# Kernel optimization log

Measured on AMD Instinct MI355X. Metric: run time of the kernel, lower is better.

The kernel has to match this reference:

```python
import jax, jax.numpy as jnp
import numpy as np

N = 50000          # nodes
E = 600000         # edges
D_IN = 256         # input_feat_dim
H1 = 128           # hidden_dim1
H2 = 64            # hidden_dim2
DK = 64            # trs_depth (total key/value depth)
HEADS = 2


def setup_inputs() -> dict:
    key = jax.random.key(0)
    ks = jax.random.split(key, 12)
    inp = {
        "ns_emb": jax.random.normal(ks[0], (N, D_IN), dtype=jnp.float32),
        "edge_rows": jax.random.randint(ks[1], (E,), 0, N, dtype=jnp.int32),
        "edge_cols": jax.random.randint(ks[2], (E,), 0, N, dtype=jnp.int32),
        "edge_vals": jax.random.uniform(ks[3], (E,), dtype=jnp.float32),
        "condition": jax.random.normal(ks[4], (1, 128, H1), dtype=jnp.float32),
        # GCN linear weights (bias=False), stored [in, out]
        "W_hidden": jax.random.normal(ks[5], (D_IN, H1), dtype=jnp.float32) / np.sqrt(D_IN),
        "W_mu": jax.random.normal(ks[6], (H1, H2), dtype=jnp.float32) / np.sqrt(H1),
        "W_var": jax.random.normal(ks[7], (H1, H2), dtype=jnp.float32) / np.sqrt(H1),
        # MultiHeadAttention (bias-free) projections
        "Wq": jax.random.normal(ks[8], (H1, DK), dtype=jnp.float32) / np.sqrt(H1),
        "Wk": jax.random.normal(ks[9], (H1, DK), dtype=jnp.float32) / np.sqrt(H1),
        "Wv": jax.random.normal(ks[10], (H1, DK), dtype=jnp.float32) / np.sqrt(H1),
        "Wo": jax.random.normal(ks[11], (DK, H1), dtype=jnp.float32) / np.sqrt(DK),
    }
    return inp


def _spmm(rows, cols, vals, x):
    # sparse [N,N] @ x  via gather + segment-sum over COO edges
    gathered = vals[:, None] * x[cols]            # [E, d]
    return jax.ops.segment_sum(gathered, rows, num_segments=N)


def _gcn(x, W, rows, cols, vals):
    # dropout is identity in eval mode
    support = jax.nn.leaky_relu(x @ W)            # [N, out]
    out = _spmm(rows, cols, vals, support)        # [N, out]
    return jax.nn.leaky_relu(out)


def _mha(q, kv, Wq, Wk, Wv, Wo):
    # MoEL-style MultiHeadAttention, bias-free, no mask/dropout
    B, Lq, _ = q.shape
    Lk = kv.shape[1]
    dk = DK // HEADS
    Q = (q @ Wq).reshape(B, Lq, HEADS, dk).transpose(0, 2, 1, 3) * (dk ** -0.5)
    K = (kv @ Wk).reshape(B, Lk, HEADS, dk).transpose(0, 2, 1, 3)
    V = (kv @ Wv).reshape(B, Lk, HEADS, dk).transpose(0, 2, 1, 3)
    logits = jnp.einsum("bhqd,bhkd->bhqk", Q, K)
    w = jax.nn.softmax(logits, axis=-1)
    ctx = jnp.einsum("bhqk,bhkd->bhqd", w, V)
    ctx = ctx.transpose(0, 2, 1, 3).reshape(B, Lq, DK)
    return ctx @ Wo, w


def reference(ns_emb, edge_rows, edge_cols, edge_vals, condition,
              W_hidden, W_mu, W_var, Wq, Wk, Wv, Wo):
    hidden = _gcn(ns_emb, W_hidden, edge_rows, edge_cols, edge_vals)   # [N, H1]
    attended, _ = _mha(hidden[None], condition, Wq, Wk, Wv, Wo)        # [1, N, H1]
    h = attended[0]
    mu = _gcn(h, W_mu, edge_rows, edge_cols, edge_vals)                # [N, H2]
    var = _gcn(h, W_var, edge_rows, edge_cols, edge_vals)              # [N, H2]
    return mu, var
```

## Files before the change

kernel.cpp:

```cpp
#include <hip/hip_runtime.h>
#include <hip/hip_bf16.h>
#include <cstdint>


typedef __attribute__((ext_vector_type(8))) short short8;
typedef __attribute__((ext_vector_type(4))) float f32x4;

__device__ __forceinline__ unsigned short f2bf(float f) {
    unsigned int u = __builtin_bit_cast(unsigned int, f);
    u += 0x7fffu + ((u >> 16) & 1u);
    return (unsigned short)(u >> 16);
}
__device__ __forceinline__ float bf2f(unsigned short v) {
    return __builtin_bit_cast(float, (unsigned int)v << 16);
}
__device__ __forceinline__ unsigned int pk2(float a, float b) {
    unsigned int r;
    asm("v_cvt_pk_bf16_f32 %0, %1, %2" : "=v"(r) : "v"(a), "v"(b));
    return r;
}


__global__ __launch_bounds__(256) void hist_prep_kernel(
    const int* __restrict__ rows, int* __restrict__ cnt, int E, int HB,
    const float* __restrict__ Wh, const float* __restrict__ Wq,
    const float* __restrict__ cond,
    const float* __restrict__ Wk, const float* __restrict__ Wv,
    const float* __restrict__ Wo, const float* __restrict__ Wmu,
    const float* __restrict__ Wvar,
    unsigned short* __restrict__ WhT, unsigned short* __restrict__ WqT,
    unsigned short* __restrict__ Ktt, unsigned short* __restrict__ Vt,
    unsigned short* __restrict__ WomT)
{
    const int t = threadIdx.x;
    if ((int)blockIdx.x < HB) {
        int i = blockIdx.x * 256 + t;
        if (i < E) atomicAdd(&cnt[rows[i]], 1);
        return;
    }
    const int bid = blockIdx.x - HB;
    if (bid < 160) {
        int idx = bid * 256 + t;
        if (idx < 32768) {
            int n = idx & 127, k = idx >> 7;
            WhT[n * 256 + k] = f2bf(Wh[k * 128 + n]);
        } else {
            int i = idx - 32768, n = i & 63, k = i >> 6;
            WqT[n * 128 + k] = f2bf(Wq[k * 64 + n]);
        }
    } else if (bid < 224) {
        int b2 = bid - 160;
        __shared__ float c[2][128];
        c[t >> 7][t & 127] = cond[b2 * 256 + t];
        __syncthreads();
        int j = b2 * 2 + (t >> 7);
        int tl = t & 127;
        const float* W = (tl < 64) ? Wk : Wv;
        int col = tl & 63;
        float acc = 0.f;
#pragma unroll 8
        for (int k = 0; k < 128; ++k) acc = fmaf(c[t >> 7][k], W[k * 64 + col], acc);
        int h = col >> 5, d = col & 31;
        if (tl < 64) Ktt[((size_t)h * 128 + j) * 32 + d] = f2bf(acc * 0.17677669529663687f);
        else         Vt[((size_t)h * 32 + d) * 128 + j] = f2bf(acc);
    } else {
        int wb = bid - 224;
        __shared__ float WoTl[128 * 65];
#pragma unroll
        for (int i = 0; i < 32; ++i) {
            int idx = t + 256 * i;
            int d = idx >> 7, k = idx & 127;
            WoTl[k * 65 + d] = Wo[idx];
        }
        __syncthreads();
        int o = wb * 256 + t;
        int d = o & 63, n = o >> 6;
        const float* W = (n < 64) ? Wmu : Wvar;
        int j = n & 63;
        float acc = 0.f;
#pragma unroll 8
        for (int k = 0; k < 128; ++k) acc = fmaf(WoTl[k * 65 + d], W[k * 64 + j], acc);
        WomT[n * 64 + d] = f2bf(acc);
    }
}


__global__ __launch_bounds__(256) void scan_fused_kernel(
    const int* __restrict__ cnt, int* __restrict__ bsum, int* __restrict__ flag,
    int* __restrict__ row_start, int* __restrict__ cursor, int N, int E)
{
    __shared__ int sh[256];
    const int t = threadIdx.x, b = blockIdx.x;
    const int i = b * 256 + t;
    int v = (i < N) ? cnt[i] : 0;
    sh[t] = v;
    __syncthreads();
    for (int off = 1; off < 256; off <<= 1) {
        int x = (t >= off) ? sh[t - off] : 0;
        __syncthreads();
        sh[t] += x;
        __syncthreads();
    }
    const int incl = sh[t];
    const int aggregate = sh[255];

    if (t == 255) {
        __hip_atomic_store(&bsum[b], aggregate, __ATOMIC_RELAXED, __HIP_MEMORY_SCOPE_AGENT);
        __hip_atomic_store(&flag[b], 1, __ATOMIC_RELEASE, __HIP_MEMORY_SCOPE_AGENT);
    }

    int acc = 0;
    if (t < b) {
        while (__hip_atomic_load(&flag[t], __ATOMIC_ACQUIRE, __HIP_MEMORY_SCOPE_AGENT) == 0) {}
        acc = __hip_atomic_load(&bsum[t], __ATOMIC_RELAXED, __HIP_MEMORY_SCOPE_AGENT);
    }
    __syncthreads();
    sh[t] = acc;
    __syncthreads();
    for (int off = 128; off > 0; off >>= 1) {
        if (t < off) sh[t] += sh[t + off];
        __syncthreads();
    }
    const int boff = sh[0];
    if (i < N) {
        int w = incl - v + boff;
        row_start[i] = w;
        cursor[i] = w;
    }
    if (b == 0 && t == 0) row_start[N] = E;
}

__global__ void scatter_kernel(const int* __restrict__ rows, const int* __restrict__ colsIn,
                               const float* __restrict__ valsIn, int* __restrict__ cursor,
                               int2* __restrict__ pack, int E) {
    int i = blockIdx.x * blockDim.x + threadIdx.x;
    if (i < E) {
        int r = rows[i];
        int p = atomicAdd(&cursor[r], 1);
        pack[p] = make_int2(colsIn[i], __float_as_int(valsIn[i]));
    }
}


__global__ __launch_bounds__(256) void gcn1_gemm(
    const float* __restrict__ A, const unsigned short* __restrict__ BT,
    unsigned short* __restrict__ C, int M)
{
    __shared__ unsigned short As[128][72];
    __shared__ unsigned short Bs[128][72];

    const int tid = threadIdx.x;
    const int lane = tid & 63, wave = tid >> 6;
    const int wm = wave & 1, wn = wave >> 1;
    const int quad = lane >> 4, l16 = lane & 15;
    const int r0 = blockIdx.x * 128;

    f32x4 acc[4][4];
#pragma unroll
    for (int mt = 0; mt < 4; ++mt)
#pragma unroll
        for (int nt = 0; nt < 4; ++nt)
#pragma unroll
            for (int r = 0; r < 4; ++r) acc[mt][nt][r] = 0.f;

    for (int kc = 0; kc < 256; kc += 64) {
#pragma unroll
        for (int i = 0; i < 8; ++i) {
            int f = tid + 256 * i;
            int row = f >> 4, kq = (f & 15) << 2;
            int gr = r0 + row;
            if (gr >= M) gr = M - 1;
            float4 v = *reinterpret_cast<const float4*>(&A[(size_t)gr * 256 + kc + kq]);
            unsigned int lo = pk2(v.x, v.y), hi = pk2(v.z, v.w);
            *reinterpret_cast<uint2*>(&As[row][kq]) = make_uint2(lo, hi);
        }
#pragma unroll
        for (int i = 0; i < 4; ++i) {
            int f = tid + 256 * i;
            int n = f >> 3, k8 = (f & 7) << 3;
            *reinterpret_cast<short8*>(&Bs[n][k8]) =
                *reinterpret_cast<const short8*>(&BT[(size_t)n * 256 + kc + k8]);
        }
        __syncthreads();

#pragma unroll
        for (int ks = 0; ks < 2; ++ks) {
            const int koff = ks * 32 + quad * 8;
            short8 a[4], b[4];
#pragma unroll
            for (int mt = 0; mt < 4; ++mt)
                a[mt] = *reinterpret_cast<const short8*>(&As[wm * 64 + mt * 16 + l16][koff]);
#pragma unroll
            for (int nt = 0; nt < 4; ++nt)
                b[nt] = *reinterpret_cast<const short8*>(&Bs[wn * 64 + nt * 16 + l16][koff]);
#pragma unroll
            for (int mt = 0; mt < 4; ++mt)
#pragma unroll
                for (int nt = 0; nt < 4; ++nt)
                    acc[mt][nt] = __builtin_amdgcn_mfma_f32_16x16x32_bf16(
                        a[mt], b[nt], acc[mt][nt], 0, 0, 0);
        }
        __syncthreads();
    }

#pragma unroll
    for (int mt = 0; mt < 4; ++mt)
#pragma unroll
        for (int nt = 0; nt < 4; ++nt) {
            int gc = wn * 64 + nt * 16 + l16;
#pragma unroll
            for (int r = 0; r < 4; ++r) {
                int gr = r0 + wm * 64 + mt * 16 + quad * 4 + r;
                if (gr < M) {
                    float v = acc[mt][nt][r];
                    v = v > 0.f ? v : 0.01f * v;
                    C[(size_t)gr * 128 + gc] = f2bf(v);
                }
            }
        }
}


__global__ __launch_bounds__(256) void attn_muvar_kernel(
    const unsigned short* __restrict__ hidden,
    const unsigned short* __restrict__ WqT,
    const unsigned short* __restrict__ Ktt,
    const unsigned short* __restrict__ Vt,
    const unsigned short* __restrict__ WomT,
    unsigned short* __restrict__ muvar,
    int M)
{
    __shared__ unsigned short Qs[4][16 * 72];
    __shared__ unsigned short Ps[4][16 * 136];
    __shared__ unsigned short Csh[4][16 * 72];

    const int tid = threadIdx.x;
    const int lane = tid & 63, wave = tid >> 6;
    const int quad = lane >> 4, l16 = lane & 15;

    const int strip = blockIdx.x * 4 + wave;
    const int base = strip * 16;
    if (base >= M) return;
    int qrow = base + l16;
    if (qrow >= M) qrow = M - 1;

    unsigned short* Q  = &Qs[wave][0];
    unsigned short* P  = &Ps[wave][0];
    unsigned short* Cl = &Csh[wave][0];

    {
        f32x4 qacc[4];
#pragma unroll
        for (int mt = 0; mt < 4; ++mt)
#pragma unroll
            for (int r = 0; r < 4; ++r) qacc[mt][r] = 0.f;

        short8 hb[4];
#pragma unroll
        for (int ks = 0; ks < 4; ++ks)
            hb[ks] = *reinterpret_cast<const short8*>(
                &hidden[(size_t)qrow * 128 + ks * 32 + quad * 8]);
#pragma unroll
        for (int mt = 0; mt < 4; ++mt)
#pragma unroll
            for (int ks = 0; ks < 4; ++ks) {
                short8 a = *reinterpret_cast<const short8*>(
                    &WqT[(size_t)(mt * 16 + l16) * 128 + ks * 32 + quad * 8]);
                qacc[mt] = __builtin_amdgcn_mfma_f32_16x16x32_bf16(a, hb[ks], qacc[mt], 0, 0, 0);
            }
#pragma unroll
        for (int mt = 0; mt < 4; ++mt) {
            uint2 w;
            w.x = pk2(qacc[mt][0], qacc[mt][1]);
            w.y = pk2(qacc[mt][2], qacc[mt][3]);
            *reinterpret_cast<uint2*>(&Q[l16 * 72 + mt * 16 + quad * 4]) = w;
        }
    }

    f32x4 ctv[2][2];
#pragma unroll
    for (int h = 0; h < 2; ++h)
#pragma unroll
        for (int mt = 0; mt < 2; ++mt)
#pragma unroll
            for (int r = 0; r < 4; ++r) ctv[h][mt][r] = 0.f;

#pragma unroll
    for (int h = 0; h < 2; ++h) {
        f32x4 st[8];
        short8 qb = *reinterpret_cast<const short8*>(&Q[l16 * 72 + h * 32 + quad * 8]);
#pragma unroll
        for (int mt = 0; mt < 8; ++mt) {
            short8 a = *reinterpret_cast<const short8*>(
                &Ktt[(size_t)h * 4096 + (mt * 16 + l16) * 32 + quad * 8]);
            f32x4 z; z[0] = 0.f; z[1] = 0.f; z[2] = 0.f; z[3] = 0.f;
            st[mt] = __builtin_amdgcn_mfma_f32_16x16x32_bf16(a, qb, z, 0, 0, 0);
        }

        float mx = st[0][0];
#pragma unroll
        for (int mt = 0; mt < 8; ++mt)
#pragma unroll
            for (int r = 0; r < 4; ++r) mx = fmaxf(mx, st[mt][r]);
        mx = fmaxf(mx, __shfl_xor(mx, 16, 64));
        mx = fmaxf(mx, __shfl_xor(mx, 32, 64));
        float s = 0.f;
#pragma unroll
        for (int mt = 0; mt < 8; ++mt)
#pragma unroll
            for (int r = 0; r < 4; ++r) {
                float e = __expf(st[mt][r] - mx);
                st[mt][r] = e;
                s += e;
            }
        s += __shfl_xor(s, 16, 64);
        s += __shfl_xor(s, 32, 64);
        float inv = 1.0f / s;

#pragma unroll
        for (int mt = 0; mt < 8; ++mt) {
            uint2 w;
            w.x = pk2(st[mt][0] * inv, st[mt][1] * inv);
            w.y = pk2(st[mt][2] * inv, st[mt][3] * inv);
            *reinterpret_cast<uint2*>(&P[l16 * 136 + mt * 16 + quad * 4]) = w;
        }

#pragma unroll
        for (int ks = 0; ks < 4; ++ks) {
            short8 pb = *reinterpret_cast<const short8*>(&P[l16 * 136 + ks * 32 + quad * 8]);
#pragma unroll
            for (int mt = 0; mt < 2; ++mt) {
                short8 a = *reinterpret_cast<const short8*>(
                    &Vt[(size_t)h * 4096 + (mt * 16 + l16) * 128 + ks * 32 + quad * 8]);
                ctv[h][mt] = __builtin_amdgcn_mfma_f32_16x16x32_bf16(a, pb, ctv[h][mt], 0, 0, 0);
            }
        }
    }

#pragma unroll
    for (int h = 0; h < 2; ++h)
#pragma unroll
        for (int mt = 0; mt < 2; ++mt) {
            uint2 w;
            w.x = pk2(ctv[h][mt][0], ctv[h][mt][1]);
            w.y = pk2(ctv[h][mt][2], ctv[h][mt][3]);
            *reinterpret_cast<uint2*>(&Cl[l16 * 72 + h * 32 + mt * 16 + quad * 4]) = w;
        }

    {
        f32x4 mv[8];
#pragma unroll
        for (int mt = 0; mt < 8; ++mt)
#pragma unroll
            for (int r = 0; r < 4; ++r) mv[mt][r] = 0.f;
        short8 cb[2];
#pragma unroll
        for (int ks = 0; ks < 2; ++ks)
            cb[ks] = *reinterpret_cast<const short8*>(&Cl[l16 * 72 + ks * 32 + quad * 8]);
#pragma unroll
        for (int mt = 0; mt < 8; ++mt)
#pragma unroll
            for (int ks = 0; ks < 2; ++ks) {
                short8 a = *reinterpret_cast<const short8*>(
                    &WomT[(size_t)(mt * 16 + l16) * 64 + ks * 32 + quad * 8]);
                mv[mt] = __builtin_amdgcn_mfma_f32_16x16x32_bf16(a, cb[ks], mv[mt], 0, 0, 0);
            }
        if (base + l16 < M) {
#pragma unroll
            for (int mt = 0; mt < 8; ++mt) {
                float v0 = mv[mt][0], v1 = mv[mt][1], v2 = mv[mt][2], v3 = mv[mt][3];
                v0 = v0 > 0.f ? v0 : 0.01f * v0;
                v1 = v1 > 0.f ? v1 : 0.01f * v1;
                v2 = v2 > 0.f ? v2 : 0.01f * v2;
                v3 = v3 > 0.f ? v3 : 0.01f * v3;
                uint2 w;
                w.x = pk2(v0, v1);
                w.y = pk2(v2, v3);
                *reinterpret_cast<uint2*>(
                    &muvar[(size_t)(base + l16) * 128 + mt * 16 + quad * 4]) = w;
            }
        }
    }
}


template<bool SPLIT, typename OT>
__global__ __launch_bounds__(256) void spmm_kernel(
    const int* __restrict__ row_start, const int2* __restrict__ pack,
    const unsigned short* __restrict__ X,
    OT* __restrict__ out0, OT* __restrict__ out1, int N)
{
    const int wave = threadIdx.x >> 6, lane = threadIdx.x & 63;
    const int r = blockIdx.x * 4 + wave;
    if (r >= N) return;
    const int s = __builtin_amdgcn_readfirstlane(row_start[r]);
    const int e = __builtin_amdgcn_readfirstlane(row_start[r + 1]);
    const int fo = lane * 2;

    float ax[16], ay[16];
#pragma unroll
    for (int k = 0; k < 16; ++k) { ax[k] = 0.f; ay[k] = 0.f; }

    for (int i = s; i < e; i += 16) {
        int2 p[16];
        unsigned int x[16];
#pragma unroll
        for (int k = 0; k < 16; ++k) {
            int idx = i + k;
            p[k] = pack[idx < e ? idx : e - 1];
        }
#pragma unroll
        for (int k = 0; k < 16; ++k)
            x[k] = *reinterpret_cast<const unsigned int*>(&X[(size_t)p[k].x * 128 + fo]);
#pragma unroll
        for (int k = 0; k < 16; ++k) {
            float v = (i + k < e) ? __int_as_float(p[k].y) : 0.f;
            ax[k] = fmaf(v, bf2f((unsigned short)x[k]), ax[k]);
            ay[k] = fmaf(v, bf2f((unsigned short)(x[k] >> 16)), ay[k]);
        }
    }

    float ox = (((ax[0] + ax[1]) + (ax[2] + ax[3])) + ((ax[4] + ax[5]) + (ax[6] + ax[7]))) +
               (((ax[8] + ax[9]) + (ax[10] + ax[11])) + ((ax[12] + ax[13]) + (ax[14] + ax[15])));
    float oy = (((ay[0] + ay[1]) + (ay[2] + ay[3])) + ((ay[4] + ay[5]) + (ay[6] + ay[7]))) +
               (((ay[8] + ay[9]) + (ay[10] + ay[11])) + ((ay[12] + ay[13]) + (ay[14] + ay[15])));
    ox = ox > 0.f ? ox : 0.01f * ox;
    oy = oy > 0.f ? oy : 0.01f * oy;

    if constexpr (!SPLIT) {
        unsigned int w = (unsigned int)f2bf(ox) | ((unsigned int)f2bf(oy) << 16);
        *reinterpret_cast<unsigned int*>(&out0[(size_t)r * 128 + fo]) = w;
    } else {
        if (lane < 32) {
            *reinterpret_cast<float2*>(&out0[(size_t)r * 64 + fo]) = make_float2(ox, oy);
        } else {
            *reinterpret_cast<float2*>(&out1[(size_t)r * 64 + (fo - 64)]) = make_float2(ox, oy);
        }
    }
}


extern "C" void kernel_launch(void* const* d_in, const int* in_sizes, int n_in,
                              void* d_out, int out_size, void* d_ws, size_t ws_size,
                              hipStream_t stream)
{
    const float* ns_emb   = (const float*)d_in[0];
    const int*   erows    = (const int*)d_in[1];
    const int*   ecols    = (const int*)d_in[2];
    const float* evals    = (const float*)d_in[3];
    const float* cond     = (const float*)d_in[4];
    const float* W_hidden = (const float*)d_in[5];
    const float* W_mu     = (const float*)d_in[6];
    const float* W_var    = (const float*)d_in[7];
    const float* Wq       = (const float*)d_in[8];
    const float* Wk       = (const float*)d_in[9];
    const float* Wv       = (const float*)d_in[10];
    const float* Wo       = (const float*)d_in[11];

    const int N = in_sizes[0] / 256;
    const int E = in_sizes[1];

    typedef unsigned short bf16;
    uint8_t* p = (uint8_t*)d_ws;
    auto alloc = [&](size_t bytes) {
        uint8_t* r = p;
        p += (bytes + 255) & ~(size_t)255;
        return r;
    };
    bf16* support1 = (bf16*)alloc(sizeof(bf16) * (size_t)N * 128);
    bf16* hidden   = (bf16*)alloc(sizeof(bf16) * (size_t)N * 128);
    bf16* muvarb   = (bf16*)alloc(sizeof(bf16) * (size_t)N * 128);
    bf16* Ktt      = (bf16*)alloc(sizeof(bf16) * 2 * 128 * 32);
    bf16* Vt       = (bf16*)alloc(sizeof(bf16) * 2 * 32 * 128);
    bf16* WhT      = (bf16*)alloc(sizeof(bf16) * 128 * 256);
    bf16* WqT      = (bf16*)alloc(sizeof(bf16) * 64 * 128);
    bf16* WomT     = (bf16*)alloc(sizeof(bf16) * 128 * 64);
    int*  cnt      = (int*)alloc(sizeof(int) * N);
    int*  flag     = (int*)alloc(sizeof(int) * 256);
    int*  bsum     = (int*)alloc(sizeof(int) * 256);
    int*  row_start= (int*)alloc(sizeof(int) * (N + 1));
    int*  cursor   = (int*)alloc(sizeof(int) * N);
    int2* pack     = (int2*)alloc(sizeof(int2) * E);

    const int HB = (E + 255) / 256;
    const int nb = (N + 255) / 256;

    size_t zbytes = (size_t)((uint8_t*)flag - (uint8_t*)cnt) + sizeof(int) * 256;
    hipMemsetAsync(cnt, 0, zbytes, stream);

    hist_prep_kernel<<<HB + 256, 256, 0, stream>>>(erows, cnt, E, HB,
                                                   W_hidden, Wq, cond, Wk, Wv,
                                                   Wo, W_mu, W_var,
                                                   WhT, WqT, Ktt, Vt, WomT);

    scan_fused_kernel<<<nb, 256, 0, stream>>>(cnt, bsum, flag, row_start, cursor, N, E);

    scatter_kernel<<<HB, 256, 0, stream>>>(erows, ecols, evals, cursor, pack, E);

    const int mb128 = (N + 127) / 128;
    gcn1_gemm<<<mb128, 256, 0, stream>>>(ns_emb, WhT, support1, N);

    const int sblocks = (N + 3) / 4;
    spmm_kernel<false, bf16><<<sblocks, 256, 0, stream>>>(
        row_start, pack, support1, hidden, nullptr, N);

    const int strips = (N + 15) / 16;
    const int ablocks = (strips + 3) / 4;
    attn_muvar_kernel<<<ablocks, 256, 0, stream>>>(hidden, WqT, Ktt, Vt,
                                                   WomT, muvarb, N);

    spmm_kernel<true, float><<<sblocks, 256, 0, stream>>>(
        row_start, pack, muvarb, (float*)d_out, (float*)d_out + (size_t)N * 64, N);
}
```

Measured before the change: 286.3 us.

## Fuse edge scatter into GEMM launch, batch edges per thread, split SpMM tail

The CSR scatter becomes extra blocks at the front of the first GCN GEMM launch, so the two independent phases run in one grid and can overlap. Histogram and scatter blocks now each handle four edges per thread, which cuts the block count and issues the loads before the atomics. The SpMM inner loop drops from 16-wide to 8-wide, with an unmasked main loop and a masked tail, which lowers register pressure and removes per-edge bounds checks. The risk is that the shared-memory GEMM footprint now also applies to the scatter blocks, and the narrower unroll leaves fewer gathers in flight.

```diff
diff --git a/kernel.cpp b/kernel.cpp
--- a/kernel.cpp
+++ b/kernel.cpp
@@ -22,7 +22,7 @@
 
 
 __global__ __launch_bounds__(256) void hist_prep_kernel(
-    const int* __restrict__ rows, int* __restrict__ cnt, int E, int HB,
+    const int* __restrict__ rows, int* __restrict__ cnt, int E, int SC,
     const float* __restrict__ Wh, const float* __restrict__ Wq,
     const float* __restrict__ cond,
     const float* __restrict__ Wk, const float* __restrict__ Wv,
@@ -33,12 +33,22 @@
     unsigned short* __restrict__ WomT)
 {
     const int t = threadIdx.x;
-    if ((int)blockIdx.x < HB) {
-        int i = blockIdx.x * 256 + t;
-        if (i < E) atomicAdd(&cnt[rows[i]], 1);
+    if ((int)blockIdx.x < SC) {
+        const int T = SC * 256;
+        const int i0 = blockIdx.x * 256 + t;
+        int r[4]; bool ok[4];
+#pragma unroll
+        for (int k = 0; k < 4; ++k) {
+            int idx = i0 + k * T;
+            ok[k] = idx < E;
+            r[k] = rows[ok[k] ? idx : 0];
+        }
+#pragma unroll
+        for (int k = 0; k < 4; ++k)
+            if (ok[k]) atomicAdd(&cnt[r[k]], 1);
         return;
     }
-    const int bid = blockIdx.x - HB;
+    const int bid = blockIdx.x - SC;
     if (bid < 160) {
         int idx = bid * 256 + t;
         if (idx < 32768) {
@@ -130,19 +140,11 @@
     if (b == 0 && t == 0) row_start[N] = E;
 }
 
-__global__ void scatter_kernel(const int* __restrict__ rows, const int* __restrict__ colsIn,
-                               const float* __restrict__ valsIn, int* __restrict__ cursor,
-                               int2* __restrict__ pack, int E) {
-    int i = blockIdx.x * blockDim.x + threadIdx.x;
-    if (i < E) {
-        int r = rows[i];
-        int p = atomicAdd(&cursor[r], 1);
-        pack[p] = make_int2(colsIn[i], __float_as_int(valsIn[i]));
-    }
-}
-
-
-__global__ __launch_bounds__(256) void gcn1_gemm(
+
+__global__ __launch_bounds__(256) void scatter_gcn1_kernel(
+    const int* __restrict__ rows, const int* __restrict__ colsIn,
+    const float* __restrict__ valsIn, int* __restrict__ cursor,
+    int2* __restrict__ pack, int E, int SC,
     const float* __restrict__ A, const unsigned short* __restrict__ BT,
     unsigned short* __restrict__ C, int M)
 {
@@ -150,10 +152,34 @@
     __shared__ unsigned short Bs[128][72];
 
     const int tid = threadIdx.x;
+
+    if ((int)blockIdx.x < SC) {
+        const int T = SC * 256;
+        const int i0 = blockIdx.x * 256 + tid;
+        int r[4], c[4], vb[4]; bool ok[4];
+#pragma unroll
+        for (int k = 0; k < 4; ++k) {
+            int idx = i0 + k * T;
+            ok[k] = idx < E;
+            int safe = ok[k] ? idx : 0;
+            r[k] = rows[safe];
+            c[k] = colsIn[safe];
+            vb[k] = __float_as_int(valsIn[safe]);
+        }
+        int pos[4];
+#pragma unroll
+        for (int k = 0; k < 4; ++k)
+            if (ok[k]) pos[k] = atomicAdd(&cursor[r[k]], 1);
+#pragma unroll
+        for (int k = 0; k < 4; ++k)
+            if (ok[k]) pack[pos[k]] = make_int2(c[k], vb[k]);
+        return;
+    }
+
     const int lane = tid & 63, wave = tid >> 6;
     const int wm = wave & 1, wn = wave >> 1;
     const int quad = lane >> 4, l16 = lane & 15;
-    const int r0 = blockIdx.x * 128;
+    const int r0 = ((int)blockIdx.x - SC) * 128;
 
     f32x4 acc[4][4];
 #pragma unroll
@@ -393,37 +419,51 @@
     const int wave = threadIdx.x >> 6, lane = threadIdx.x & 63;
     const int r = blockIdx.x * 4 + wave;
     if (r >= N) return;
-    const int s = __builtin_amdgcn_readfirstlane(row_start[r]);
-    const int e = __builtin_amdgcn_readfirstlane(row_start[r + 1]);
+    int s = __builtin_amdgcn_readfirstlane(row_start[r]);
+    int e = __builtin_amdgcn_readfirstlane(row_start[r + 1]);
     const int fo = lane * 2;
 
-    float ax[16], ay[16];
-#pragma unroll
-    for (int k = 0; k < 16; ++k) { ax[k] = 0.f; ay[k] = 0.f; }
-
-    for (int i = s; i < e; i += 16) {
-        int2 p[16];
-        unsigned int x[16];
-#pragma unroll
-        for (int k = 0; k < 16; ++k) {
+    float ax[8], ay[8];
+#pragma unroll
+    for (int k = 0; k < 8; ++k) { ax[k] = 0.f; ay[k] = 0.f; }
+
+    int i = s;
+    for (; i + 8 <= e; i += 8) {
+        int2 p[8];
+        unsigned int x[8];
+#pragma unroll
+        for (int k = 0; k < 8; ++k) p[k] = pack[i + k];
+#pragma unroll
+        for (int k = 0; k < 8; ++k)
+            x[k] = *reinterpret_cast<const unsigned int*>(&X[(size_t)p[k].x * 128 + fo]);
+#pragma unroll
+        for (int k = 0; k < 8; ++k) {
+            float v = __int_as_float(p[k].y);
+            ax[k] = fmaf(v, bf2f((unsigned short)x[k]), ax[k]);
+            ay[k] = fmaf(v, bf2f((unsigned short)(x[k] >> 16)), ay[k]);
+        }
+    }
+    if (i < e) {
+        int2 p[8];
+        unsigned int x[8];
+#pragma unroll
+        for (int k = 0; k < 8; ++k) {
             int idx = i + k;
             p[k] = pack[idx < e ? idx : e - 1];
         }
 #pragma unroll
-        for (int k = 0; k < 16; ++k)
+        for (int k = 0; k < 8; ++k)
             x[k] = *reinterpret_cast<const unsigned int*>(&X[(size_t)p[k].x * 128 + fo]);
 #pragma unroll
-        for (int k = 0; k < 16; ++k) {
+        for (int k = 0; k < 8; ++k) {
             float v = (i + k < e) ? __int_as_float(p[k].y) : 0.f;
             ax[k] = fmaf(v, bf2f((unsigned short)x[k]), ax[k]);
             ay[k] = fmaf(v, bf2f((unsigned short)(x[k] >> 16)), ay[k]);
         }
     }
 
-    float ox = (((ax[0] + ax[1]) + (ax[2] + ax[3])) + ((ax[4] + ax[5]) + (ax[6] + ax[7]))) +
-               (((ax[8] + ax[9]) + (ax[10] + ax[11])) + ((ax[12] + ax[13]) + (ax[14] + ax[15])));
-    float oy = (((ay[0] + ay[1]) + (ay[2] + ay[3])) + ((ay[4] + ay[5]) + (ay[6] + ay[7]))) +
-               (((ay[8] + ay[9]) + (ay[10] + ay[11])) + ((ay[12] + ay[13]) + (ay[14] + ay[15])));
+    float ox = ((ax[0] + ax[1]) + (ax[2] + ax[3])) + ((ax[4] + ax[5]) + (ax[6] + ax[7]));
+    float oy = ((ay[0] + ay[1]) + (ay[2] + ay[3])) + ((ay[4] + ay[5]) + (ay[6] + ay[7]));
     ox = ox > 0.f ? ox : 0.01f * ox;
     oy = oy > 0.f ? oy : 0.01f * oy;
 
@@ -482,23 +522,23 @@
     int*  cursor   = (int*)alloc(sizeof(int) * N);
     int2* pack     = (int2*)alloc(sizeof(int2) * E);
 
-    const int HB = (E + 255) / 256;
+    const int SC = (E + 1023) / 1024;
     const int nb = (N + 255) / 256;
+    const int mb128 = (N + 127) / 128;
 
     size_t zbytes = (size_t)((uint8_t*)flag - (uint8_t*)cnt) + sizeof(int) * 256;
     hipMemsetAsync(cnt, 0, zbytes, stream);
 
-    hist_prep_kernel<<<HB + 256, 256, 0, stream>>>(erows, cnt, E, HB,
+    hist_prep_kernel<<<SC + 256, 256, 0, stream>>>(erows, cnt, E, SC,
                                                    W_hidden, Wq, cond, Wk, Wv,
                                                    Wo, W_mu, W_var,
                                                    WhT, WqT, Ktt, Vt, WomT);
 
     scan_fused_kernel<<<nb, 256, 0, stream>>>(cnt, bsum, flag, row_start, cursor, N, E);
 
-    scatter_kernel<<<HB, 256, 0, stream>>>(erows, ecols, evals, cursor, pack, E);
-
-    const int mb128 = (N + 127) / 128;
-    gcn1_gemm<<<mb128, 256, 0, stream>>>(ns_emb, WhT, support1, N);
+    scatter_gcn1_kernel<<<SC + mb128, 256, 0, stream>>>(
+        erows, ecols, evals, cursor, pack, E, SC,
+        ns_emb, WhT, support1, N);
 
     const int sblocks = (N + 3) / 4;
     spmm_kernel<false, bf16><<<sblocks, 256, 0, stream>>>(
```

New measurement: 276.9 us. 1.03x faster.
